# Kernel optimization log

Measured on AMD Instinct MI355X. Metric: run time of the kernel, lower is better.

## Reference

```python
import jax, jax.numpy as jnp
import numpy as np

N = 100000      # nodes
E = 1600000     # edges (before self-loops)
F_IN = 256      # num_features
H = 128         # hidden (fixed in source)
C = 47          # num_classes


def setup_inputs() -> dict:
    key = jax.random.key(0)
    k1, k2, k3, k4 = jax.random.split(key, 4)
    x = jax.random.normal(k1, (N, F_IN), dtype=jnp.float32)
    edge_index = jax.random.randint(k2, (2, E), 0, N, dtype=jnp.int32)
    # Glorot-ish init for GCN weights, zero bias (PyG default)
    W1 = jax.random.normal(k3, (F_IN, H), dtype=jnp.float32) * (1.0 / np.sqrt(F_IN))
    b1 = jnp.zeros((H,), dtype=jnp.float32)
    W2 = jax.random.normal(k4, (H, C), dtype=jnp.float32) * (1.0 / np.sqrt(H))
    b2 = jnp.zeros((C,), dtype=jnp.float32)
    return {"x": x, "edge_index": edge_index, "W1": W1, "b1": b1, "W2": W2, "b2": b2}


def gcn_conv(x, W, b, src, dst, n):
    """PyG GCNConv: linear transform, then D^{-1/2} A_hat D^{-1/2} aggregation.
    src/dst already include self-loops. Aggregates messages onto dst."""
    xw = x @ W  # [n, out]
    deg = jax.ops.segment_sum(jnp.ones(dst.shape[0], xw.dtype), dst, num_segments=n)
    dinv = jnp.where(deg > 0, jax.lax.rsqrt(deg), 0.0)
    norm = dinv[src] * dinv[dst]                 # [E_tot]
    msg = xw[src] * norm[:, None]                # gather + scale, [E_tot, out]
    out = jax.ops.segment_sum(msg, dst, num_segments=n)  # scatter-add
    return out + b


def reference(x, edge_index, W1, b1, W2, b2):
    n = x.shape[0]
    loops = jnp.arange(n, dtype=edge_index.dtype)
    src = jnp.concatenate([edge_index[0], loops])
    dst = jnp.concatenate([edge_index[1], loops])
    h = jax.nn.relu(gcn_conv(x, W1, b1, src, dst, n))
    # dropout is identity at inference (training=False)
    out = gcn_conv(h, W2, b2, src, dst, n)
    return jax.nn.log_softmax(out, axis=1)
```

## Files before the change

kernel.cpp:

```cpp
#include <hip/hip_runtime.h>
#include <math.h>

#define N_NODES 100000
#define N_EDGES 1600000
#define F_INN   256
#define HID     128
#define NCLS    47

#define SCAN_CHUNK 1024
#define N_SBLOCKS ((N_NODES + SCAN_CHUNK - 1) / SCAN_CHUNK)

typedef __attribute__((ext_vector_type(8))) short bf16x8;
typedef __attribute__((ext_vector_type(4))) float f32x4;
typedef __attribute__((ext_vector_type(2))) float f32x2;

__device__ __forceinline__ unsigned bf16pack(float a, float b) {
    unsigned ua = __float_as_uint(a), ub = __float_as_uint(b);
    ua = (ua + 0x7FFFu + ((ua >> 16) & 1u)) >> 16;
    ub = (ub + 0x7FFFu + ((ub >> 16) & 1u)) >> 16;
    return ua | (ub << 16);
}
__device__ __forceinline__ float2 bf16unpack(unsigned v) {
    return make_float2(__uint_as_float(v << 16), __uint_as_float(v & 0xFFFF0000u));
}

__device__ __forceinline__ unsigned fp8enc(float f) {
    unsigned u = __float_as_uint(f);
    unsigned r = u + 0x7FFFFu + ((u >> 20) & 1u);
    unsigned exp = (r >> 23) & 0xFFu;
    unsigned s = (u >> 24) & 0x80u;
    if (exp < 121u) return s;
    if (exp > 135u) return s | 0x7Eu;
    return s | ((exp - 120u) << 3) | ((r >> 20) & 7u);
}

#if __has_builtin(__builtin_amdgcn_cvt_pk_f32_fp8) && __has_builtin(__builtin_amdgcn_cvt_f32_fp8)
#define HWCVT 1
#endif

__device__ __forceinline__ void fp8dec4(unsigned v, float& a, float& b, float& c, float& d) {
#ifdef HWCVT
    f32x2 lo = __builtin_amdgcn_cvt_pk_f32_fp8((int)v, false);
    f32x2 hi = __builtin_amdgcn_cvt_pk_f32_fp8((int)v, true);
    a = lo[0]; b = lo[1]; c = hi[0]; d = hi[1];
#else
    unsigned p0 = v & 0xFFFFu, p1 = v >> 16;
    unsigned m0 = ((p0 & 0x7Fu) << 4) + ((p0 & 0x7F00u) << 12) + 0x3C003C00u;
    unsigned g0 = ((p0 & 0x80u) << 8) | ((p0 & 0x8000u) << 16);
    unsigned b0 = m0 | g0;
    unsigned m1 = ((p1 & 0x7Fu) << 4) + ((p1 & 0x7F00u) << 12) + 0x3C003C00u;
    unsigned g1 = ((p1 & 0x80u) << 8) | ((p1 & 0x8000u) << 16);
    unsigned b1_ = m1 | g1;
    a = __uint_as_float(b0 << 16); b = __uint_as_float(b0 & 0xFFFF0000u);
    c = __uint_as_float(b1_ << 16); d = __uint_as_float(b1_ & 0xFFFF0000u);
#endif
}

__global__ void k_init(int* cnt) {
    int i = blockIdx.x * blockDim.x + threadIdx.x;
    if (i < N_NODES) cnt[i] = 0;
}

__global__ __launch_bounds__(256) void k_count(const int4* __restrict__ dst4, int* cnt,
                                               uchar4* __restrict__ rank4) {
    int t = blockIdx.x * blockDim.x + threadIdx.x;
    if (t < N_EDGES / 4) {
        int4 d = dst4[t];
        unsigned r0 = atomicAdd(&cnt[d.x], 1);
        unsigned r1 = atomicAdd(&cnt[d.y], 1);
        unsigned r2 = atomicAdd(&cnt[d.z], 1);
        unsigned r3 = atomicAdd(&cnt[d.w], 1);
        rank4[t] = make_uchar4((unsigned char)r0, (unsigned char)r1,
                               (unsigned char)r2, (unsigned char)r3);
    }
}

__global__ __launch_bounds__(256) void k_scan_part(const int* __restrict__ cnt,
                                                   int* __restrict__ bsum) {
    int b = blockIdx.x, t = threadIdx.x;
    int base = b * SCAN_CHUNK;
    int local = 0;
#pragma unroll
    for (int u = 0; u < 4; u++) {
        int idx = base + u * 256 + t;
        if (idx < N_NODES) local += cnt[idx];
    }
#pragma unroll
    for (int off = 32; off >= 1; off >>= 1) local += __shfl_down(local, off, 64);
    __shared__ int red[4];
    if ((t & 63) == 0) red[t >> 6] = local;
    __syncthreads();
    if (t == 0) bsum[b] = red[0] + red[1] + red[2] + red[3];
}

__global__ void k_scan_top(const int* __restrict__ bsum, int* __restrict__ boff) {
    __shared__ int s[128];
    int t = threadIdx.x;
    int v = (t < N_SBLOCKS) ? bsum[t] : 0;
    s[t] = v;
    __syncthreads();
    for (int off = 1; off < 128; off <<= 1) {
        int u = (t >= off) ? s[t - off] : 0;
        __syncthreads();
        s[t] += u;
        __syncthreads();
    }
    if (t < N_SBLOCKS) boff[t] = s[t] - v;
}

__global__ __launch_bounds__(256) void k_scan_final(const int* __restrict__ cnt,
                                                    const int* __restrict__ boff,
                                                    int* __restrict__ rowptr,
                                                    float* __restrict__ dinv) {
    __shared__ int tsum[256];
    int b = blockIdx.x, t = threadIdx.x;
    int base = b * SCAN_CHUNK + t * 4;
    int c[4];
    int local = 0;
#pragma unroll
    for (int u = 0; u < 4; u++) {
        int idx = base + u;
        c[u] = (idx < N_NODES) ? cnt[idx] : 0;
        local += c[u];
    }
    tsum[t] = local;
    __syncthreads();
    for (int off = 1; off < 256; off <<= 1) {
        int u = (t >= off) ? tsum[t - off] : 0;
        __syncthreads();
        tsum[t] += u;
        __syncthreads();
    }
    int run = boff[b] + tsum[t] - local;
#pragma unroll
    for (int u = 0; u < 4; u++) {
        int idx = base + u;
        if (idx < N_NODES) {
            rowptr[idx] = run;
            dinv[idx] = rsqrtf((float)c[u] + 1.0f);
            run += c[u];
        }
    }
    if (b == 0 && t == 0) rowptr[N_NODES] = N_EDGES;
}

__global__ __launch_bounds__(256) void k_scatter(const int4* __restrict__ src4,
                                                 const int4* __restrict__ dst4,
                                                 const int* __restrict__ rowptr,
                                                 const uchar4* __restrict__ rank4,
                                                 int* __restrict__ eidx) {
    int t = blockIdx.x * blockDim.x + threadIdx.x;
    if (t < N_EDGES / 4) {
        int4 s = src4[t];
        int4 d = dst4[t];
        uchar4 r = rank4[t];
        int p0 = rowptr[d.x] + (int)r.x;
        int p1 = rowptr[d.y] + (int)r.y;
        int p2 = rowptr[d.z] + (int)r.z;
        int p3 = rowptr[d.w] + (int)r.w;
        eidx[p0] = s.x;
        eidx[p1] = s.y;
        eidx[p2] = s.z;
        eidx[p3] = s.w;
    }
}

__global__ __launch_bounds__(256) void k_prep(const float* __restrict__ W1,
                                              uint4* __restrict__ Wf) {
    int g = blockIdx.x * blockDim.x + threadIdx.x;
    if (g >= 4096) return;
    int l = g & 63;
    int kst = (g >> 6) & 7;
    int nt = g >> 9;
    int n = nt * 16 + (l & 15);
    int kb = kst * 32 + ((l >> 4) << 3);
    float v[8];
#pragma unroll
    for (int j = 0; j < 8; j++) v[j] = W1[(size_t)(kb + j) * HID + n];
    uint4 o;
    o.x = bf16pack(v[0], v[1]);
    o.y = bf16pack(v[2], v[3]);
    o.z = bf16pack(v[4], v[5]);
    o.w = bf16pack(v[6], v[7]);
    Wf[g] = o;
}

__global__ __launch_bounds__(256) void k_gemm1(const float* __restrict__ X,
                                               const uint4* __restrict__ Wf,
                                               const float* __restrict__ dinv,
                                               unsigned char* __restrict__ Y8) {
    __shared__ __align__(16) unsigned short xs[128 * 32];
    int tid = threadIdx.x;
    int lane = tid & 63, w = tid >> 6;
    int wr = w >> 1, wc = w & 1;
    int row0 = blockIdx.x * 128;

    f32x4 acc[4][4];
#pragma unroll
    for (int i = 0; i < 4; i++)
#pragma unroll
        for (int j = 0; j < 4; j++) acc[i][j] = (f32x4){0.f, 0.f, 0.f, 0.f};

    for (int ks = 0; ks < 8; ks++) {
        int k0 = ks * 32;
#pragma unroll
        for (int u = 0; u < 4; u++) {
            int slot = u * 256 + tid;
            int r = slot >> 3, c4 = slot & 7;
            int rr = min(row0 + r, N_NODES - 1);
            float4 v = *(const float4*)&X[(size_t)rr * F_INN + k0 + c4 * 4];
            uint2 p;
            p.x = bf16pack(v.x, v.y);
            p.y = bf16pack(v.z, v.w);
            *(uint2*)&xs[r * 32 + c4 * 4] = p;
        }
        bf16x8 bfr[4];
#pragma unroll
        for (int fn = 0; fn < 4; fn++) {
            uint4 t = Wf[((wc * 4 + fn) * 8 + ks) * 64 + lane];
            bfr[fn] = *(bf16x8*)&t;
        }
        __syncthreads();
        bf16x8 afr[4];
#pragma unroll
        for (int fm = 0; fm < 4; fm++) {
            int r = wr * 64 + fm * 16 + (lane & 15);
            afr[fm] = *(const bf16x8*)&xs[r * 32 + ((lane >> 4) << 3)];
        }
#pragma unroll
        for (int fm = 0; fm < 4; fm++)
#pragma unroll
            for (int fn = 0; fn < 4; fn++)
                acc[fm][fn] = __builtin_amdgcn_mfma_f32_16x16x32_bf16(
                    bfr[fn], afr[fm], acc[fm][fn], 0, 0, 0);
        __syncthreads();
    }
#pragma unroll
    for (int fm = 0; fm < 4; fm++) {
        int row = row0 + wr * 64 + fm * 16 + (lane & 15);
        if (row < N_NODES) {
            float s = dinv[row];
            unsigned char* yrow = Y8 + (size_t)row * 128;
#pragma unroll
            for (int fn = 0; fn < 4; fn++) {
                int col = wc * 64 + fn * 16 + ((lane >> 4) << 2);
                unsigned o = fp8enc(acc[fm][fn][0] * s)
                           | (fp8enc(acc[fm][fn][1] * s) << 8)
                           | (fp8enc(acc[fm][fn][2] * s) << 16)
                           | (fp8enc(acc[fm][fn][3] * s) << 24);
                *(unsigned*)&yrow[col] = o;
            }
        }
    }
}

__global__ __launch_bounds__(256) void k_gather1(const unsigned* __restrict__ Y32,
                                                 const int* __restrict__ rowptr,
                                                 const int* __restrict__ eidx,
                                                 const float* __restrict__ dinv,
                                                 const float* __restrict__ b1,
                                                 unsigned* __restrict__ Hb) {
    int wid = (blockIdx.x * blockDim.x + threadIdx.x) >> 6;
    int lane = threadIdx.x & 63;
    int half = lane >> 5, sl = lane & 31;
    int node = wid * 2 + half;
    if (node >= N_NODES) return;

    float a0, a1, a2, a3;
    fp8dec4(Y32[(size_t)node * 32 + sl], a0, a1, a2, a3);
    int beg = rowptr[node], end = rowptr[node + 1];
    int e = beg;
    int n8 = beg + ((end - beg) & ~7);
    for (; e < n8; e += 8) {
        int j[8];
#pragma unroll
        for (int u = 0; u < 8; u++) j[u] = eidx[e + u];
        unsigned v[8];
#pragma unroll
        for (int u = 0; u < 8; u++) v[u] = Y32[(size_t)j[u] * 32 + sl];
#pragma unroll
        for (int u = 0; u < 8; u++) {
            float d0, d1, d2, d3;
            fp8dec4(v[u], d0, d1, d2, d3);
            a0 += d0; a1 += d1; a2 += d2; a3 += d3;
        }
    }
    for (; e < end; e++) {
        unsigned v = Y32[(size_t)eidx[e] * 32 + sl];
        float d0, d1, d2, d3;
        fp8dec4(v, d0, d1, d2, d3);
        a0 += d0; a1 += d1; a2 += d2; a3 += d3;
    }
    float s = dinv[node];
    float4 b = ((const float4*)b1)[sl];
    uint2 p;
    p.x = bf16pack(fmaxf(a0 * s + b.x, 0.f), fmaxf(a1 * s + b.y, 0.f));
    p.y = bf16pack(fmaxf(a2 * s + b.z, 0.f), fmaxf(a3 * s + b.w, 0.f));
    *(uint2*)&Hb[(size_t)node * 64 + sl * 2] = p;
}

__global__ __launch_bounds__(256) void k_gemm2(const unsigned* __restrict__ Hb,
                                               const float* __restrict__ W2,
                                               const float* __restrict__ dinv,
                                               unsigned char* __restrict__ Y2_8) {
    __shared__ __align__(16) float ws[128][48];
    int tid = threadIdx.x;
    for (int idx = tid; idx < 128 * 48; idx += 256) {
        int k = idx / 48, c = idx - k * 48;
        ws[k][c] = (c < NCLS) ? W2[k * NCLS + c] : 0.f;
    }
    __syncthreads();
    int row = blockIdx.x * 256 + tid;
    if (row >= N_NODES) return;
    float4 acc[12];
#pragma unroll
    for (int i = 0; i < 12; i++) acc[i] = make_float4(0.f, 0.f, 0.f, 0.f);
    const uint4* h4 = (const uint4*)(Hb + (size_t)row * 64);
    for (int kq = 0; kq < 16; kq++) {
        uint4 hv = h4[kq];
        float f[8];
        float2 f0 = bf16unpack(hv.x), f1 = bf16unpack(hv.y);
        float2 f2 = bf16unpack(hv.z), f3 = bf16unpack(hv.w);
        f[0] = f0.x; f[1] = f0.y; f[2] = f1.x; f[3] = f1.y;
        f[4] = f2.x; f[5] = f2.y; f[6] = f3.x; f[7] = f3.y;
#pragma unroll
        for (int u = 0; u < 8; u++) {
            float xv = f[u];
            int k = kq * 8 + u;
#pragma unroll
            for (int c = 0; c < 12; c++) {
                float4 w = *(const float4*)&ws[k][c * 4];
                acc[c].x += xv * w.x; acc[c].y += xv * w.y;
                acc[c].z += xv * w.z; acc[c].w += xv * w.w;
            }
        }
    }
    float s = dinv[row];
#pragma unroll
    for (int c = 0; c < 12; c++) {
        unsigned o = fp8enc(acc[c].x * s)
                   | (fp8enc(acc[c].y * s) << 8)
                   | (fp8enc(acc[c].z * s) << 16)
                   | (fp8enc(acc[c].w * s) << 24);
        *(unsigned*)&Y2_8[(size_t)row * 64 + c * 4] = o;
    }
}

__global__ __launch_bounds__(256) void k_gather2(const unsigned* __restrict__ Y2_32,
                                                 const int* __restrict__ rowptr,
                                                 const int* __restrict__ eidx,
                                                 const float* __restrict__ dinv,
                                                 const float* __restrict__ b2,
                                                 float* __restrict__ Out) {
    int wid = (blockIdx.x * blockDim.x + threadIdx.x) >> 6;
    int lane = threadIdx.x & 63;
    int q = lane >> 4, sl = lane & 15;
    int node = wid * 4 + q;
    if (node >= N_NODES) return;

    float a0, a1, a2, a3;
    fp8dec4(Y2_32[(size_t)node * 16 + sl], a0, a1, a2, a3);
    int beg = rowptr[node], end = rowptr[node + 1];
    int e = beg;
    int n8 = beg + ((end - beg) & ~7);
    for (; e < n8; e += 8) {
        int j[8];
#pragma unroll
        for (int u = 0; u < 8; u++) j[u] = eidx[e + u];
        unsigned v[8];
#pragma unroll
        for (int u = 0; u < 8; u++) v[u] = Y2_32[(size_t)j[u] * 16 + sl];
#pragma unroll
        for (int u = 0; u < 8; u++) {
            float d0, d1, d2, d3;
            fp8dec4(v[u], d0, d1, d2, d3);
            a0 += d0; a1 += d1; a2 += d2; a3 += d3;
        }
    }
    for (; e < end; e++) {
        unsigned v = Y2_32[(size_t)eidx[e] * 16 + sl];
        float d0, d1, d2, d3;
        fp8dec4(v, d0, d1, d2, d3);
        a0 += d0; a1 += d1; a2 += d2; a3 += d3;
    }
    float s = dinv[node];
    int d0i = sl * 4;
    float v0 = (d0i + 0 < NCLS) ? a0 * s + b2[d0i + 0] : -INFINITY;
    float v1 = (d0i + 1 < NCLS) ? a1 * s + b2[d0i + 1] : -INFINITY;
    float v2 = (d0i + 2 < NCLS) ? a2 * s + b2[d0i + 2] : -INFINITY;
    float v3 = (d0i + 3 < NCLS) ? a3 * s + b2[d0i + 3] : -INFINITY;
    float m = fmaxf(fmaxf(v0, v1), fmaxf(v2, v3));
#pragma unroll
    for (int off = 1; off < 16; off <<= 1) m = fmaxf(m, __shfl_xor(m, off, 16));
    float ex = 0.f;
    ex += (d0i + 0 < NCLS) ? __expf(v0 - m) : 0.f;
    ex += (d0i + 1 < NCLS) ? __expf(v1 - m) : 0.f;
    ex += (d0i + 2 < NCLS) ? __expf(v2 - m) : 0.f;
    ex += (d0i + 3 < NCLS) ? __expf(v3 - m) : 0.f;
#pragma unroll
    for (int off = 1; off < 16; off <<= 1) ex += __shfl_xor(ex, off, 16);
    float l = __logf(ex);
    float* orow = Out + (size_t)node * NCLS;
    if (d0i + 0 < NCLS) orow[d0i + 0] = v0 - m - l;
    if (d0i + 1 < NCLS) orow[d0i + 1] = v1 - m - l;
    if (d0i + 2 < NCLS) orow[d0i + 2] = v2 - m - l;
    if (d0i + 3 < NCLS) orow[d0i + 3] = v3 - m - l;
}

extern "C" void kernel_launch(void* const* d_in, const int* in_sizes, int n_in,
                              void* d_out, int out_size, void* d_ws, size_t ws_size,
                              hipStream_t stream) {
    const float* x   = (const float*)d_in[0];
    const int*   ei  = (const int*)d_in[1];
    const float* W1  = (const float*)d_in[2];
    const float* b1  = (const float*)d_in[3];
    const float* W2  = (const float*)d_in[4];
    const float* b2  = (const float*)d_in[5];
    float* out = (float*)d_out;

    const int* src = ei;
    const int* dst = ei + N_EDGES;

    char* ws = (char*)d_ws;
    unsigned char*  y8   = (unsigned char*) (ws + 0);
    unsigned*       hb   = (unsigned*)      (ws + 12800000);
    unsigned char*  y2_8 = (unsigned char*) (ws + 38400000);
    float*          dinv = (float*)         (ws + 44800000);
    int*            cnt  = (int*)           (ws + 45200000);
    int*            rowptr=(int*)           (ws + 45600000);
    int*            eidx = (int*)           (ws + 46000016);
    int*            bsum = (int*)           (ws + 52400016);
    int*            boff = (int*)           (ws + 52401040);
    unsigned char*  rank = (unsigned char*) (ws + 52402064);
    uint4*          wfrag= (uint4*)         (ws + 54002064);

    k_init<<<(N_NODES + 255) / 256, 256, 0, stream>>>(cnt);
    k_count<<<(N_EDGES / 4 + 255) / 256, 256, 0, stream>>>(
        (const int4*)dst, cnt, (uchar4*)rank);
    k_scan_part<<<N_SBLOCKS, 256, 0, stream>>>(cnt, bsum);
    k_scan_top<<<1, 128, 0, stream>>>(bsum, boff);
    k_scan_final<<<N_SBLOCKS, 256, 0, stream>>>(cnt, boff, rowptr, dinv);
    k_scatter<<<(N_EDGES / 4 + 255) / 256, 256, 0, stream>>>(
        (const int4*)src, (const int4*)dst, rowptr, (const uchar4*)rank, eidx);

    k_prep<<<16, 256, 0, stream>>>(W1, wfrag);

    k_gemm1<<<(N_NODES + 127) / 128, 256, 0, stream>>>(x, wfrag, dinv, y8);
    k_gather1<<<((N_NODES + 1) / 2 * 64 + 255) / 256, 256, 0, stream>>>(
        (const unsigned*)y8, rowptr, eidx, dinv, b1, hb);

    k_gemm2<<<(N_NODES + 255) / 256, 256, 0, stream>>>(hb, W2, dinv, y2_8);
    k_gather2<<<((N_NODES + 3) / 4 * 64 + 255) / 256, 256, 0, stream>>>(
        (const unsigned*)y2_8, rowptr, eidx, dinv, b2, out);
}
```

Measured before the change: 263.8 us.

## Fuse degree counting into GEMM1 launch by moving source-side dinv scaling to gather

GEMM1 no longer scales its output rows by dinv, so it no longer has to wait for the degree count and scan. Its blocks are interleaved with the edge-counting atomic blocks in one launch, so the compute-bound GEMM and the atomic-bound counting can overlap. In exchange, gather1 now loads dinv[j] for every neighbour and applies it with an FMA, which adds one random 4-byte load per edge. The self term is scaled by dinv[node] explicitly.

```diff
diff --git a/kernel.cpp b/kernel.cpp
--- a/kernel.cpp
+++ b/kernel.cpp
@@ -9,6 +9,8 @@
 
 #define SCAN_CHUNK 1024
 #define N_SBLOCKS ((N_NODES + SCAN_CHUNK - 1) / SCAN_CHUNK)
+#define G1_BLOCKS ((N_NODES + 127) / 128)
+#define CNT_BLOCKS ((N_EDGES / 4 + 255) / 256)
 
 typedef __attribute__((ext_vector_type(8))) short bf16x8;
 typedef __attribute__((ext_vector_type(4))) float f32x4;
@@ -59,20 +61,6 @@
 __global__ void k_init(int* cnt) {
     int i = blockIdx.x * blockDim.x + threadIdx.x;
     if (i < N_NODES) cnt[i] = 0;
-}
-
-__global__ __launch_bounds__(256) void k_count(const int4* __restrict__ dst4, int* cnt,
-                                               uchar4* __restrict__ rank4) {
-    int t = blockIdx.x * blockDim.x + threadIdx.x;
-    if (t < N_EDGES / 4) {
-        int4 d = dst4[t];
-        unsigned r0 = atomicAdd(&cnt[d.x], 1);
-        unsigned r1 = atomicAdd(&cnt[d.y], 1);
-        unsigned r2 = atomicAdd(&cnt[d.z], 1);
-        unsigned r3 = atomicAdd(&cnt[d.w], 1);
-        rank4[t] = make_uchar4((unsigned char)r0, (unsigned char)r1,
-                               (unsigned char)r2, (unsigned char)r3);
-    }
 }
 
 __global__ __launch_bounds__(256) void k_scan_part(const int* __restrict__ cnt,
@@ -185,15 +173,41 @@
     Wf[g] = o;
 }
 
-__global__ __launch_bounds__(256) void k_gemm1(const float* __restrict__ X,
-                                               const uint4* __restrict__ Wf,
-                                               const float* __restrict__ dinv,
-                                               unsigned char* __restrict__ Y8) {
+__global__ __launch_bounds__(256) void k_fusedA(const float* __restrict__ X,
+                                                const uint4* __restrict__ Wf,
+                                                unsigned char* __restrict__ Y8,
+                                                const int4* __restrict__ dst4,
+                                                int* cnt,
+                                                uchar4* __restrict__ rank4) {
     __shared__ __align__(16) unsigned short xs[128 * 32];
+    int bid = blockIdx.x;
     int tid = threadIdx.x;
+
+    int gemm_b = -1, cnt_b = -1;
+    if (bid < 2 * G1_BLOCKS) {
+        if (bid & 1) cnt_b = bid >> 1;
+        else gemm_b = bid >> 1;
+    } else {
+        cnt_b = G1_BLOCKS + (bid - 2 * G1_BLOCKS);
+    }
+
+    if (cnt_b >= 0) {
+        int t = cnt_b * 256 + tid;
+        if (t < N_EDGES / 4) {
+            int4 d = dst4[t];
+            unsigned r0 = atomicAdd(&cnt[d.x], 1);
+            unsigned r1 = atomicAdd(&cnt[d.y], 1);
+            unsigned r2 = atomicAdd(&cnt[d.z], 1);
+            unsigned r3 = atomicAdd(&cnt[d.w], 1);
+            rank4[t] = make_uchar4((unsigned char)r0, (unsigned char)r1,
+                                   (unsigned char)r2, (unsigned char)r3);
+        }
+        return;
+    }
+
     int lane = tid & 63, w = tid >> 6;
     int wr = w >> 1, wc = w & 1;
-    int row0 = blockIdx.x * 128;
+    int row0 = gemm_b * 128;
 
     f32x4 acc[4][4];
 #pragma unroll
@@ -217,8 +231,8 @@
         bf16x8 bfr[4];
 #pragma unroll
         for (int fn = 0; fn < 4; fn++) {
-            uint4 t = Wf[((wc * 4 + fn) * 8 + ks) * 64 + lane];
-            bfr[fn] = *(bf16x8*)&t;
+            uint4 t4 = Wf[((wc * 4 + fn) * 8 + ks) * 64 + lane];
+            bfr[fn] = *(bf16x8*)&t4;
         }
         __syncthreads();
         bf16x8 afr[4];
@@ -239,15 +253,14 @@
     for (int fm = 0; fm < 4; fm++) {
         int row = row0 + wr * 64 + fm * 16 + (lane & 15);
         if (row < N_NODES) {
-            float s = dinv[row];
             unsigned char* yrow = Y8 + (size_t)row * 128;
 #pragma unroll
             for (int fn = 0; fn < 4; fn++) {
                 int col = wc * 64 + fn * 16 + ((lane >> 4) << 2);
-                unsigned o = fp8enc(acc[fm][fn][0] * s)
-                           | (fp8enc(acc[fm][fn][1] * s) << 8)
-                           | (fp8enc(acc[fm][fn][2] * s) << 16)
-                           | (fp8enc(acc[fm][fn][3] * s) << 24);
+                unsigned o = fp8enc(acc[fm][fn][0])
+                           | (fp8enc(acc[fm][fn][1]) << 8)
+                           | (fp8enc(acc[fm][fn][2]) << 16)
+                           | (fp8enc(acc[fm][fn][3]) << 24);
                 *(unsigned*)&yrow[col] = o;
             }
         }
@@ -266,8 +279,10 @@
     int node = wid * 2 + half;
     if (node >= N_NODES) return;
 
-    float a0, a1, a2, a3;
-    fp8dec4(Y32[(size_t)node * 32 + sl], a0, a1, a2, a3);
+    float s = dinv[node];
+    float d0, d1, d2, d3;
+    fp8dec4(Y32[(size_t)node * 32 + sl], d0, d1, d2, d3);
+    float a0 = s * d0, a1 = s * d1, a2 = s * d2, a3 = s * d3;
     int beg = rowptr[node], end = rowptr[node + 1];
     int e = beg;
     int n8 = beg + ((end - beg) & ~7);
@@ -276,22 +291,31 @@
 #pragma unroll
         for (int u = 0; u < 8; u++) j[u] = eidx[e + u];
         unsigned v[8];
-#pragma unroll
-        for (int u = 0; u < 8; u++) v[u] = Y32[(size_t)j[u] * 32 + sl];
+        float dv[8];
 #pragma unroll
         for (int u = 0; u < 8; u++) {
-            float d0, d1, d2, d3;
+            v[u] = Y32[(size_t)j[u] * 32 + sl];
+            dv[u] = dinv[j[u]];
+        }
+#pragma unroll
+        for (int u = 0; u < 8; u++) {
             fp8dec4(v[u], d0, d1, d2, d3);
-            a0 += d0; a1 += d1; a2 += d2; a3 += d3;
+            a0 = fmaf(dv[u], d0, a0);
+            a1 = fmaf(dv[u], d1, a1);
+            a2 = fmaf(dv[u], d2, a2);
+            a3 = fmaf(dv[u], d3, a3);
         }
     }
     for (; e < end; e++) {
-        unsigned v = Y32[(size_t)eidx[e] * 32 + sl];
-        float d0, d1, d2, d3;
+        int j = eidx[e];
+        unsigned v = Y32[(size_t)j * 32 + sl];
+        float dvv = dinv[j];
         fp8dec4(v, d0, d1, d2, d3);
-        a0 += d0; a1 += d1; a2 += d2; a3 += d3;
-    }
-    float s = dinv[node];
+        a0 = fmaf(dvv, d0, a0);
+        a1 = fmaf(dvv, d1, a1);
+        a2 = fmaf(dvv, d2, a2);
+        a3 = fmaf(dvv, d3, a3);
+    }
     float4 b = ((const float4*)b1)[sl];
     uint2 p;
     p.x = bf16pack(fmaxf(a0 * s + b.x, 0.f), fmaxf(a1 * s + b.y, 0.f));
@@ -435,17 +459,17 @@
     uint4*          wfrag= (uint4*)         (ws + 54002064);
 
     k_init<<<(N_NODES + 255) / 256, 256, 0, stream>>>(cnt);
-    k_count<<<(N_EDGES / 4 + 255) / 256, 256, 0, stream>>>(
-        (const int4*)dst, cnt, (uchar4*)rank);
+    k_prep<<<16, 256, 0, stream>>>(W1, wfrag);
+
+    k_fusedA<<<2 * G1_BLOCKS + (CNT_BLOCKS - G1_BLOCKS), 256, 0, stream>>>(
+        x, wfrag, y8, (const int4*)dst, cnt, (uchar4*)rank);
+
     k_scan_part<<<N_SBLOCKS, 256, 0, stream>>>(cnt, bsum);
     k_scan_top<<<1, 128, 0, stream>>>(bsum, boff);
     k_scan_final<<<N_SBLOCKS, 256, 0, stream>>>(cnt, boff, rowptr, dinv);
-    k_scatter<<<(N_EDGES / 4 + 255) / 256, 256, 0, stream>>>(
+    k_scatter<<<CNT_BLOCKS, 256, 0, stream>>>(
         (const int4*)src, (const int4*)dst, rowptr, (const uchar4*)rank, eidx);
 
-    k_prep<<<16, 256, 0, stream>>>(W1, wfrag);
-
-    k_gemm1<<<(N_NODES + 127) / 128, 256, 0, stream>>>(x, wfrag, dinv, y8);
     k_gather1<<<((N_NODES + 1) / 2 * 64 + 255) / 256, 256, 0, stream>>>(
         (const unsigned*)y8, rowptr, eidx, dinv, b1, hb);
 
```

New measurement: 236.9 us. 1.11x faster.
